# Kernel tuning notes

Hardware: AMD Instinct MI355X
Metric: run time of the kernel (lower is better)

The kernel has to match this reference:

```python
import jax, jax.numpy as jnp
import numpy as np

EMBED = 1024
HEADS = 16
HEAD_DIM = EMBED // HEADS
N, SEQ = 8, 1024


def setup_inputs() -> dict:
    key = jax.random.key(0)
    ks = jax.random.split(key, 9)
    values = jax.random.normal(ks[0], (N, SEQ, EMBED), dtype=jnp.float32)
    keys_ = jax.random.normal(ks[1], (N, SEQ, EMBED), dtype=jnp.float32)
    query = jax.random.normal(ks[2], (N, SEQ, EMBED), dtype=jnp.float32)
    mask = jax.random.randint(ks[3], (N, 1, SEQ, SEQ), 0, 2, dtype=jnp.int32)
    s = 1.0 / np.sqrt(HEAD_DIM)
    Wv = jax.random.normal(ks[4], (HEAD_DIM, HEAD_DIM), dtype=jnp.float32) * s
    Wk = jax.random.normal(ks[5], (HEAD_DIM, HEAD_DIM), dtype=jnp.float32) * s
    Wq = jax.random.normal(ks[6], (HEAD_DIM, HEAD_DIM), dtype=jnp.float32) * s
    Wo = jax.random.normal(ks[7], (EMBED, EMBED), dtype=jnp.float32) * (1.0 / np.sqrt(EMBED))
    bo = jax.random.normal(ks[8], (EMBED,), dtype=jnp.float32) * 0.01
    return {"values": values, "keys": keys_, "query": query, "mask": mask,
            "Wv": Wv, "Wk": Wk, "Wq": Wq, "Wo": Wo, "bo": bo}


def reference(values, keys, query, mask, Wv, Wk, Wq, Wo, bo):
    n, q_len = query.shape[0], query.shape[1]
    v_len, k_len = values.shape[1], keys.shape[1]
    # reshape to (N, len, H, Dh); per-head linear projections share a (Dh,Dh) weight.
    v = values.reshape(n, v_len, HEADS, HEAD_DIM)
    k = keys.reshape(n, k_len, HEADS, HEAD_DIM)
    q = query.reshape(n, q_len, HEADS, HEAD_DIM)
    # torch Linear: x @ W.T
    v = jnp.einsum('nlhd,ed->nlhe', v, Wv)
    k = jnp.einsum('nlhd,ed->nlhe', k, Wk)
    q = jnp.einsum('nlhd,ed->nlhe', q, Wq)
    # scores (N,H,Q,K); mask BEFORE scaling, exactly as the torch module does
    att = jnp.einsum('nqhd,nkhd->nhqk', q, k)
    att = jnp.where(mask == 0, jnp.float32(-1e20), att)
    att = jax.nn.softmax(att / jnp.sqrt(jnp.float32(EMBED)), axis=3)
    out = jnp.einsum('nhql,nlhd->nqhd', att, v).reshape(n, q_len, EMBED)
    return out @ Wo.T + bo
```

## Files before the change

### kernel.cpp

```cpp
#include <hip/hip_runtime.h>
#include <hip/hip_bf16.h>

using bf16x8 = __attribute__((ext_vector_type(8))) __bf16;
using f32x4  = __attribute__((ext_vector_type(4))) float;
using f32x2  = __attribute__((ext_vector_type(2))) float;

#define NB 8
#define SEQ 1024
#define HEADS 16
#define HD 64
#define EMB 1024

#if __has_builtin(__builtin_amdgcn_exp2f)
  #define EXPD(x) __builtin_amdgcn_exp2f(x)
  #define QSCALE  0.04508422f
#else
  #define EXPD(x) __expf(x)
  #define QSCALE  0.03125f
#endif

__device__ __forceinline__ int cvtpk_bf16(float lo, float hi) {
    int r;
    asm("v_cvt_pk_bf16_f32 %0, %1, %2" : "=v"(r) : "v"(lo), "v"(hi));
    return r;
}

__device__ __forceinline__ float sel0(float e, unsigned long long m) {
    float r;
    asm("v_cndmask_b32 %0, 0, %1, %2" : "=v"(r) : "v"(e), "s"(m));
    return r;
}

__device__ __forceinline__ void gld16(const __bf16* g, __bf16* l) {
    __builtin_amdgcn_global_load_lds((const __attribute__((address_space(1))) void*)g,
                                     (__attribute__((address_space(3))) void*)l, 16, 0, 0);
}

__global__ __launch_bounds__(256) void mask_perm(const int* __restrict__ mask,
                                                 unsigned long long* __restrict__ mq)
{
    const int t = threadIdx.x, w = t >> 6, lane = t & 63, quad = lane >> 4, lq = lane & 15;
    const int bx = blockIdx.x;
    const int n = blockIdx.y;
    const int qg = bx >> 5, g = (bx >> 4) & 1, kc = bx & 15;
    const int q = qg * 128 + g * 64 + w * 16 + lq;
    const int* mrow = mask + ((size_t)n * SEQ + q) * SEQ + kc * 64 + quad * 4;
    unsigned long long* dst = mq + ((size_t)(((n * 8 + qg) * 4 + w) * 2 + g) * 16 + kc) * 16;
    #pragma unroll
    for (int kt = 0; kt < 4; ++kt)
        #pragma unroll
        for (int r = 0; r < 4; ++r) {
            unsigned long long b = __ballot(mrow[kt * 16 + r] != 0);
            if (lane == 0) dst[kt * 4 + r] = b;
        }
}

__global__ __launch_bounds__(256, 4) void proj_mfma(
    const float* __restrict__ q_in, const float* __restrict__ k_in, const float* __restrict__ v_in,
    const float* __restrict__ Wq, const float* __restrict__ Wk, const float* __restrict__ Wv,
    __bf16* __restrict__ qp, __bf16* __restrict__ kp, __bf16* __restrict__ vpt)
{
    const int z = blockIdx.z;
    const float* X  = (z == 0) ? q_in : (z == 1) ? k_in : v_in;
    const float* Wf = (z == 0) ? Wq   : (z == 1) ? Wk   : Wv;

    __shared__ __align__(16) __bf16 Wb[64 * 72];
    __shared__ __align__(16) __bf16 Xb[64 * 72];
    const int t = threadIdx.x;
    const int nh = blockIdx.y, n = nh >> 4, h = nh & 15;
    const int l0 = blockIdx.x * 64;
    for (int i = t; i < 4096; i += 256)
        Wb[(i >> 6) * 72 + (i & 63)] = (__bf16)Wf[i];
    {
        const int row = t >> 2, seg = (t & 3) * 16;
        const float* src = X + ((size_t)(n * SEQ + l0 + row)) * EMB + h * 64 + seg;
        union { __bf16 b[16]; uint4 u[2]; } tmp;
        #pragma unroll
        for (int jj = 0; jj < 4; ++jj) {
            float4 f = ((const float4*)src)[jj];
            tmp.b[jj*4+0] = (__bf16)f.x; tmp.b[jj*4+1] = (__bf16)f.y;
            tmp.b[jj*4+2] = (__bf16)f.z; tmp.b[jj*4+3] = (__bf16)f.w;
        }
        *(uint4*)&Xb[row * 72 + seg]     = tmp.u[0];
        *(uint4*)&Xb[row * 72 + seg + 8] = tmp.u[1];
    }
    __syncthreads();
    const int w = t >> 6, lane = t & 63, quad = lane >> 4, lr = lane & 15;
    bf16x8 af[2];
    #pragma unroll
    for (int ks = 0; ks < 2; ++ks)
        af[ks] = *(const bf16x8*)&Xb[(w * 16 + lr) * 72 + ks * 32 + quad * 8];
    const f32x4 zero4 = {0.f, 0.f, 0.f, 0.f};
    f32x4 acc[4];
    #pragma unroll
    for (int et = 0; et < 4; ++et) {
        acc[et] = zero4;
        #pragma unroll
        for (int ks = 0; ks < 2; ++ks) {
            bf16x8 bfrag = *(const bf16x8*)&Wb[(et * 16 + lr) * 72 + ks * 32 + quad * 8];
            acc[et] = __builtin_amdgcn_mfma_f32_16x16x32_bf16(af[ks], bfrag, acc[et], 0, 0, 0);
        }
    }
    if (z == 0) {
        #pragma unroll
        for (int et = 0; et < 4; ++et) acc[et] *= QSCALE;
    }
    __syncthreads();
    if (z < 2) {
        #pragma unroll
        for (int et = 0; et < 4; ++et)
            #pragma unroll
            for (int rr = 0; rr < 4; ++rr)
                Xb[(w * 16 + quad * 4 + rr) * 72 + et * 16 + lr] = (__bf16)acc[et][rr];
        __syncthreads();
        const int row = t >> 2, seg = (t & 3) * 16;
        uint4 a = *(uint4*)&Xb[row * 72 + seg];
        uint4 b = *(uint4*)&Xb[row * 72 + seg + 8];
        __bf16* outp = (z == 0) ? qp : kp;
        __bf16* dst = outp + (size_t)nh * 65536 + (size_t)(l0 + row) * 64 + seg;
        *(uint4*)&dst[0] = a;
        *(uint4*)&dst[8] = b;
    } else {
        #pragma unroll
        for (int et = 0; et < 4; ++et)
            #pragma unroll
            for (int rr = 0; rr < 4; ++rr)
                Xb[(et * 16 + lr) * 72 + w * 16 + quad * 4 + rr] = (__bf16)acc[et][rr];
        __syncthreads();
        const int e = t >> 2, seg = (t & 3) * 16;
        uint4 a = *(uint4*)&Xb[e * 72 + seg];
        uint4 b = *(uint4*)&Xb[e * 72 + seg + 8];
        __bf16* dst = vpt + (size_t)nh * 65536 + (size_t)e * SEQ + l0 + seg;
        *(uint4*)&dst[0] = a;
        *(uint4*)&dst[8] = b;
    }
}

__global__ __launch_bounds__(256, 4) void attn_mfma(
    const __bf16* __restrict__ qp, const __bf16* __restrict__ kp, const __bf16* __restrict__ vpt,
    const unsigned long long* __restrict__ mq, __bf16* __restrict__ attn_out)
{
    __shared__ __align__(16) __bf16 KV[2][2][64 * 64];
    const int t = threadIdx.x, w = t >> 6, lane = t & 63, quad = lane >> 4, lr = lane & 15;
    const int bid = blockIdx.x;
    const int nh = bid & 127, qg = bid >> 7;
    const int n = nh >> 4, h = nh & 15;
    const int q0 = qg * 128;
    const __bf16* Q  = qp  + (size_t)nh * 65536;
    const __bf16* K  = kp  + (size_t)nh * 65536;
    const __bf16* VT = vpt + (size_t)nh * 65536;

    const int wu = __builtin_amdgcn_readfirstlane(w);
    const unsigned long long* mq_w = mq + (size_t)((n * 8 + qg) * 4 + wu) * 512;

    int qrow[2];
    bf16x8 qf[2][2];
    #pragma unroll
    for (int g = 0; g < 2; ++g) {
        qrow[g] = q0 + g * 64 + w * 16 + lr;
        qf[g][0] = *(const bf16x8*)&Q[(size_t)qrow[g] * 64 + quad * 8];
        qf[g][1] = *(const bf16x8*)&Q[(size_t)qrow[g] * 64 + 32 + quad * 8];
    }

    const int srow = t >> 3, sc8 = t & 7;
    const int sswz = (sc8 ^ (srow & 7)) * 8;
    const int kofs = srow * 64 + sswz;
    const int vofs = srow * SEQ + sswz;

    auto issue = [&](int kc) {
        const int b = kc & 1;
        __bf16* kb = (__bf16*)&KV[b][0][0];
        __bf16* vb = (__bf16*)&KV[b][1][0];
        const __bf16* ksrc = K  + (size_t)kc * 4096 + kofs;
        const __bf16* vsrc = VT + (size_t)kc * 64   + vofs;
        gld16(ksrc,            kb + t * 8);
        gld16(ksrc + 32 * 64,  kb + t * 8 + 2048);
        gld16(vsrc,            vb + t * 8);
        gld16(vsrc + 32 * SEQ, vb + t * 8 + 2048);
    };

    const int s0 = ((quad ^ (lr & 7))) * 8;
    const int s1 = s0 ^ 32;

    const f32x4 zero4 = {0.f, 0.f, 0.f, 0.f};
    f32x4 O[2][4];
    #pragma unroll
    for (int g = 0; g < 2; ++g)
        #pragma unroll
        for (int mt = 0; mt < 4; ++mt) O[g][mt] = zero4;
    f32x2 lp2[2] = {{0.f, 0.f}, {0.f, 0.f}};

    issue(0);
    for (int kc = 0; kc < 16; ++kc) {
        __syncthreads();
        if (kc + 1 < 16) issue(kc + 1);
        const __bf16* Kb = (const __bf16*)&KV[kc & 1][0][0];
        const __bf16* Vb = (const __bf16*)&KV[kc & 1][1][0];

        f32x4 S[2][4];
        #pragma unroll
        for (int g = 0; g < 2; ++g)
            #pragma unroll
            for (int kt = 0; kt < 4; ++kt) S[g][kt] = zero4;
        __builtin_amdgcn_s_setprio(1);
        #pragma unroll
        for (int kt = 0; kt < 4; ++kt) {
            bf16x8 kf0 = *(const bf16x8*)&Kb[(kt * 16 + lr) * 64 + s0];
            bf16x8 kf1 = *(const bf16x8*)&Kb[(kt * 16 + lr) * 64 + s1];
            S[0][kt] = __builtin_amdgcn_mfma_f32_16x16x32_bf16(kf0, qf[0][0], S[0][kt], 0, 0, 0);
            S[1][kt] = __builtin_amdgcn_mfma_f32_16x16x32_bf16(kf0, qf[1][0], S[1][kt], 0, 0, 0);
            S[0][kt] = __builtin_amdgcn_mfma_f32_16x16x32_bf16(kf1, qf[0][1], S[0][kt], 0, 0, 0);
            S[1][kt] = __builtin_amdgcn_mfma_f32_16x16x32_bf16(kf1, qf[1][1], S[1][kt], 0, 0, 0);
        }
        __builtin_amdgcn_s_setprio(0);

        bf16x8 pf[2][2];
        #pragma unroll
        for (int g = 0; g < 2; ++g) {
            const unsigned long long* Mg = mq_w + g * 256 + kc * 16;
            float ev[16];
            #pragma unroll
            for (int kt = 0; kt < 4; ++kt)
                #pragma unroll
                for (int r = 0; r < 4; ++r)
                    ev[kt * 4 + r] = sel0(EXPD(S[g][kt][r]), Mg[kt * 4 + r]);
            #pragma unroll
            for (int i = 0; i < 8; ++i) {
                f32x2 p2 = {ev[2 * i], ev[2 * i + 1]};
                lp2[g] += p2;
            }
            #pragma unroll
            for (int ks = 0; ks < 2; ++ks) {
                const int ka = (2 * ks) * 4, kb2 = (2 * ks + 1) * 4;
                int d0 = cvtpk_bf16(ev[ka + 0], ev[ka + 1]);
                int d1 = cvtpk_bf16(ev[ka + 2], ev[ka + 3]);
                int d2 = cvtpk_bf16(ev[kb2 + 0], ev[kb2 + 1]);
                int d3 = cvtpk_bf16(ev[kb2 + 2], ev[kb2 + 3]);
                asm("v_permlane32_swap_b32 %0, %1" : "+v"(d0), "+v"(d2));
                asm("v_permlane16_swap_b32 %0, %1" : "+v"(d0), "+v"(d2));
                asm("v_permlane32_swap_b32 %0, %1" : "+v"(d1), "+v"(d3));
                asm("v_permlane16_swap_b32 %0, %1" : "+v"(d1), "+v"(d3));
                union { int di[4]; bf16x8 v; } pb;
                pb.di[0] = d0; pb.di[1] = d1; pb.di[2] = d2; pb.di[3] = d3;
                pf[g][ks] = pb.v;
            }
        }

        __builtin_amdgcn_s_setprio(1);
        #pragma unroll
        for (int ks = 0; ks < 2; ++ks) {
            const int sv = ks ? s1 : s0;
            #pragma unroll
            for (int mt = 0; mt < 4; ++mt) {
                bf16x8 vf = *(const bf16x8*)&Vb[(mt * 16 + lr) * 64 + sv];
                O[0][mt] = __builtin_amdgcn_mfma_f32_16x16x32_bf16(vf, pf[0][ks], O[0][mt], 0, 0, 0);
                O[1][mt] = __builtin_amdgcn_mfma_f32_16x16x32_bf16(vf, pf[1][ks], O[1][mt], 0, 0, 0);
            }
        }
        __builtin_amdgcn_s_setprio(0);
    }
    #pragma unroll
    for (int g = 0; g < 2; ++g) {
        float l = lp2[g].x + lp2[g].y;
        l += __shfl_xor(l, 16, 64);
        l += __shfl_xor(l, 32, 64);
        const float linv = 1.0f / l;
        #pragma unroll
        for (int mt = 0; mt < 4; ++mt) {
            union { __bf16 b[4]; uint2 u; } pk;
            #pragma unroll
            for (int r = 0; r < 4; ++r) pk.b[r] = (__bf16)(O[g][mt][r] * linv);
            *(uint2*)&attn_out[((size_t)n * SEQ + qrow[g]) * EMB + h * 64 + mt * 16 + quad * 4] = pk.u;
        }
    }
}

__global__ __launch_bounds__(256) void cvt_wo(const float* __restrict__ Wo, __bf16* __restrict__ Wob)
{
    int i = blockIdx.x * 256 + threadIdx.x;
    float4 f = *(const float4*)&Wo[(size_t)i * 4];
    union { __bf16 b[4]; uint2 u; } tmp;
    tmp.b[0] = (__bf16)f.x; tmp.b[1] = (__bf16)f.y; tmp.b[2] = (__bf16)f.z; tmp.b[3] = (__bf16)f.w;
    *(uint2*)&Wob[(size_t)i * 4] = tmp.u;
}

__global__ __launch_bounds__(256, 4) void out_gemm_mfma(
    const __bf16* __restrict__ A, const __bf16* __restrict__ B,
    const float* __restrict__ bo, float* __restrict__ out)
{
    __shared__ __align__(16) __bf16 As[64 * 40];
    __shared__ __align__(16) __bf16 Bs[128 * 40];
    const int t = threadIdx.x, w = t >> 6, lane = t & 63, quad = lane >> 4, lr = lane & 15;
    const int wr = (w >> 1) * 32, wc = (w & 1) * 64;
    const int r0 = blockIdx.y * 64, e0 = blockIdx.x * 128;
    const f32x4 zero4 = {0.f, 0.f, 0.f, 0.f};
    f32x4 acc[2][4];
    #pragma unroll
    for (int mt = 0; mt < 2; ++mt)
        #pragma unroll
        for (int nt = 0; nt < 4; ++nt) acc[mt][nt] = zero4;
    for (int k0 = 0; k0 < 1024; k0 += 32) {
        __syncthreads();
        {
            int row = t >> 2, c8 = t & 3;
            *(uint4*)&As[row * 40 + c8 * 8] =
                *(const uint4*)&A[(size_t)(r0 + row) * EMB + k0 + c8 * 8];
        }
        for (int c = t; c < 512; c += 256) {
            int row = c >> 2, c8 = c & 3;
            *(uint4*)&Bs[row * 40 + c8 * 8] =
                *(const uint4*)&B[(size_t)(e0 + row) * EMB + k0 + c8 * 8];
        }
        __syncthreads();
        bf16x8 af[2], bf[4];
        #pragma unroll
        for (int mt = 0; mt < 2; ++mt)
            af[mt] = *(const bf16x8*)&As[(wr + mt * 16 + lr) * 40 + quad * 8];
        #pragma unroll
        for (int nt = 0; nt < 4; ++nt)
            bf[nt] = *(const bf16x8*)&Bs[(wc + nt * 16 + lr) * 40 + quad * 8];
        #pragma unroll
        for (int mt = 0; mt < 2; ++mt)
            #pragma unroll
            for (int nt = 0; nt < 4; ++nt)
                acc[mt][nt] = __builtin_amdgcn_mfma_f32_16x16x32_bf16(af[mt], bf[nt], acc[mt][nt], 0, 0, 0);
    }
    float bv[4];
    #pragma unroll
    for (int nt = 0; nt < 4; ++nt) bv[nt] = bo[e0 + wc + nt * 16 + lr];
    #pragma unroll
    for (int mt = 0; mt < 2; ++mt)
        #pragma unroll
        for (int nt = 0; nt < 4; ++nt)
            #pragma unroll
            for (int rr = 0; rr < 4; ++rr)
                out[(size_t)(r0 + wr + mt * 16 + quad * 4 + rr) * EMB + e0 + wc + nt * 16 + lr] =
                    acc[mt][nt][rr] + bv[nt];
}

extern "C" void kernel_launch(void* const* d_in, const int* in_sizes, int n_in,
                              void* d_out, int out_size, void* d_ws, size_t ws_size,
                              hipStream_t stream) {
    const float* values = (const float*)d_in[0];
    const float* keys   = (const float*)d_in[1];
    const float* query  = (const float*)d_in[2];
    const int*   mask   = (const int*)d_in[3];
    const float* Wv     = (const float*)d_in[4];
    const float* Wk     = (const float*)d_in[5];
    const float* Wq     = (const float*)d_in[6];
    const float* Wo     = (const float*)d_in[7];
    const float* bo     = (const float*)d_in[8];
    float* out = (float*)d_out;

    const size_t per = (size_t)NB * HEADS * SEQ * HD;
    __bf16* qp   = (__bf16*)d_ws;
    __bf16* kp   = qp + per;
    __bf16* vpt  = kp + per;
    __bf16* attn = vpt + per;
    __bf16* Wob  = attn + (size_t)NB * SEQ * EMB;
    unsigned long long* maskq = (unsigned long long*)(Wob + (size_t)EMB * EMB);

    mask_perm<<<dim3(256, NB), 256, 0, stream>>>(mask, maskq);
    proj_mfma<<<dim3(16, 128, 3), 256, 0, stream>>>(query, keys, values, Wq, Wk, Wv, qp, kp, vpt);
    cvt_wo<<<1024, 256, 0, stream>>>(Wo, Wob);
    attn_mfma<<<1024, 256, 0, stream>>>(qp, kp, vpt, maskq, attn);
    out_gemm_mfma<<<dim3(EMB / 128, NB * SEQ / 64), 256, 0, stream>>>(attn, Wob, bo, out);
}
```

Before: 278.2 us.

## Stage mask via LDS, compute softmax row sums with MFMA, pipeline output GEMM

The mask_perm kernel now loads a 128x64 int tile into shared memory with coalesced 16-byte loads before doing the ballots, replacing strided per-lane global reads and halving the grid. In the attention kernel, softmax row sums are accumulated with an extra MFMA against a ones vector instead of vector adds plus cross-lane shuffles, and the zero-init of S is folded into the first MFMA. The output GEMM switches to double-buffered, swizzled direct global-to-LDS loads with a K-step of 64 and lowers occupancy to 3 blocks per CU. Summing the bf16-rounded probabilities changes the normalization slightly, and the larger LDS footprint reduces occupancy.

```diff
diff --git a/kernel.cpp b/kernel.cpp
--- a/kernel.cpp
+++ b/kernel.cpp
@@ -3,7 +3,6 @@
 
 using bf16x8 = __attribute__((ext_vector_type(8))) __bf16;
 using f32x4  = __attribute__((ext_vector_type(4))) float;
-using f32x2  = __attribute__((ext_vector_type(2))) float;
 
 #define NB 8
 #define SEQ 1024
@@ -39,20 +38,30 @@
 __global__ __launch_bounds__(256) void mask_perm(const int* __restrict__ mask,
                                                  unsigned long long* __restrict__ mq)
 {
+    __shared__ __align__(16) int Ms[128 * 68];
     const int t = threadIdx.x, w = t >> 6, lane = t & 63, quad = lane >> 4, lq = lane & 15;
-    const int bx = blockIdx.x;
     const int n = blockIdx.y;
-    const int qg = bx >> 5, g = (bx >> 4) & 1, kc = bx & 15;
-    const int q = qg * 128 + g * 64 + w * 16 + lq;
-    const int* mrow = mask + ((size_t)n * SEQ + q) * SEQ + kc * 64 + quad * 4;
-    unsigned long long* dst = mq + ((size_t)(((n * 8 + qg) * 4 + w) * 2 + g) * 16 + kc) * 16;
-    #pragma unroll
-    for (int kt = 0; kt < 4; ++kt)
-        #pragma unroll
-        for (int r = 0; r < 4; ++r) {
-            unsigned long long b = __ballot(mrow[kt * 16 + r] != 0);
-            if (lane == 0) dst[kt * 4 + r] = b;
-        }
+    const int qg = blockIdx.x >> 4, kc = blockIdx.x & 15;
+    const int* src = mask + ((size_t)n * SEQ + qg * 128) * SEQ + kc * 64;
+    #pragma unroll
+    for (int i = 0; i < 8; ++i) {
+        const int c = t + i * 256, row = c >> 4, seg = c & 15;
+        uint4 v = *(const uint4*)&src[(size_t)row * SEQ + seg * 4];
+        *(uint4*)&Ms[row * 68 + seg * 4] = v;
+    }
+    __syncthreads();
+    #pragma unroll
+    for (int g = 0; g < 2; ++g) {
+        const int row = (g * 64 + w * 16 + lq) * 68 + quad * 4;
+        unsigned long long* dst = mq + ((size_t)(((n * 8 + qg) * 4 + w) * 2 + g) * 16 + kc) * 16;
+        #pragma unroll
+        for (int kt = 0; kt < 4; ++kt)
+            #pragma unroll
+            for (int r = 0; r < 4; ++r) {
+                unsigned long long b = __ballot(Ms[row + kt * 16 + r] != 0);
+                if (lane == 0) dst[kt * 4 + r] = b;
+            }
+    }
 }
 
 __global__ __launch_bounds__(256, 4) void proj_mfma(
@@ -162,6 +171,10 @@
         qf[g][1] = *(const bf16x8*)&Q[(size_t)qrow[g] * 64 + 32 + quad * 8];
     }
 
+    bf16x8 onesf;
+    #pragma unroll
+    for (int i = 0; i < 8; ++i) onesf[i] = (__bf16)1.0f;
+
     const int srow = t >> 3, sc8 = t & 7;
     const int sswz = (sc8 ^ (srow & 7)) * 8;
     const int kofs = srow * 64 + sswz;
@@ -184,11 +197,13 @@
 
     const f32x4 zero4 = {0.f, 0.f, 0.f, 0.f};
     f32x4 O[2][4];
-    #pragma unroll
-    for (int g = 0; g < 2; ++g)
+    f32x4 Lacc[2];
+    #pragma unroll
+    for (int g = 0; g < 2; ++g) {
+        Lacc[g] = zero4;
         #pragma unroll
         for (int mt = 0; mt < 4; ++mt) O[g][mt] = zero4;
-    f32x2 lp2[2] = {{0.f, 0.f}, {0.f, 0.f}};
+    }
 
     issue(0);
     for (int kc = 0; kc < 16; ++kc) {
@@ -198,17 +213,13 @@
         const __bf16* Vb = (const __bf16*)&KV[kc & 1][1][0];
 
         f32x4 S[2][4];
-        #pragma unroll
-        for (int g = 0; g < 2; ++g)
-            #pragma unroll
-            for (int kt = 0; kt < 4; ++kt) S[g][kt] = zero4;
         __builtin_amdgcn_s_setprio(1);
         #pragma unroll
         for (int kt = 0; kt < 4; ++kt) {
             bf16x8 kf0 = *(const bf16x8*)&Kb[(kt * 16 + lr) * 64 + s0];
             bf16x8 kf1 = *(const bf16x8*)&Kb[(kt * 16 + lr) * 64 + s1];
-            S[0][kt] = __builtin_amdgcn_mfma_f32_16x16x32_bf16(kf0, qf[0][0], S[0][kt], 0, 0, 0);
-            S[1][kt] = __builtin_amdgcn_mfma_f32_16x16x32_bf16(kf0, qf[1][0], S[1][kt], 0, 0, 0);
+            S[0][kt] = __builtin_amdgcn_mfma_f32_16x16x32_bf16(kf0, qf[0][0], zero4, 0, 0, 0);
+            S[1][kt] = __builtin_amdgcn_mfma_f32_16x16x32_bf16(kf0, qf[1][0], zero4, 0, 0, 0);
             S[0][kt] = __builtin_amdgcn_mfma_f32_16x16x32_bf16(kf1, qf[0][1], S[0][kt], 0, 0, 0);
             S[1][kt] = __builtin_amdgcn_mfma_f32_16x16x32_bf16(kf1, qf[1][1], S[1][kt], 0, 0, 0);
         }
@@ -224,11 +235,6 @@
                 #pragma unroll
                 for (int r = 0; r < 4; ++r)
                     ev[kt * 4 + r] = sel0(EXPD(S[g][kt][r]), Mg[kt * 4 + r]);
-            #pragma unroll
-            for (int i = 0; i < 8; ++i) {
-                f32x2 p2 = {ev[2 * i], ev[2 * i + 1]};
-                lp2[g] += p2;
-            }
             #pragma unroll
             for (int ks = 0; ks < 2; ++ks) {
                 const int ka = (2 * ks) * 4, kb2 = (2 * ks + 1) * 4;
@@ -250,6 +256,8 @@
         #pragma unroll
         for (int ks = 0; ks < 2; ++ks) {
             const int sv = ks ? s1 : s0;
+            Lacc[0] = __builtin_amdgcn_mfma_f32_16x16x32_bf16(onesf, pf[0][ks], Lacc[0], 0, 0, 0);
+            Lacc[1] = __builtin_amdgcn_mfma_f32_16x16x32_bf16(onesf, pf[1][ks], Lacc[1], 0, 0, 0);
             #pragma unroll
             for (int mt = 0; mt < 4; ++mt) {
                 bf16x8 vf = *(const bf16x8*)&Vb[(mt * 16 + lr) * 64 + sv];
@@ -261,10 +269,7 @@
     }
     #pragma unroll
     for (int g = 0; g < 2; ++g) {
-        float l = lp2[g].x + lp2[g].y;
-        l += __shfl_xor(l, 16, 64);
-        l += __shfl_xor(l, 32, 64);
-        const float linv = 1.0f / l;
+        const float linv = 1.0f / Lacc[g][0];
         #pragma unroll
         for (int mt = 0; mt < 4; ++mt) {
             union { __bf16 b[4]; uint2 u; } pk;
@@ -284,46 +289,61 @@
     *(uint2*)&Wob[(size_t)i * 4] = tmp.u;
 }
 
-__global__ __launch_bounds__(256, 4) void out_gemm_mfma(
+__global__ __launch_bounds__(256, 3) void out_gemm_mfma(
     const __bf16* __restrict__ A, const __bf16* __restrict__ B,
     const float* __restrict__ bo, float* __restrict__ out)
 {
-    __shared__ __align__(16) __bf16 As[64 * 40];
-    __shared__ __align__(16) __bf16 Bs[128 * 40];
+    __shared__ __align__(16) __bf16 AB[2][(64 + 128) * 64];
     const int t = threadIdx.x, w = t >> 6, lane = t & 63, quad = lane >> 4, lr = lane & 15;
     const int wr = (w >> 1) * 32, wc = (w & 1) * 64;
     const int r0 = blockIdx.y * 64, e0 = blockIdx.x * 128;
+
+    const int srow = t >> 3, sj = t & 7;
+    const int sswz = (sj ^ (srow & 7)) * 8;
+
+    auto issue = [&](int st) {
+        __bf16* buf = (__bf16*)&AB[st & 1][0];
+        const __bf16* as = A + (size_t)(r0 + srow) * EMB + st * 64 + sswz;
+        const __bf16* bs = B + (size_t)(e0 + srow) * EMB + st * 64 + sswz;
+        gld16(as,            buf + t * 8);
+        gld16(as + 32 * EMB, buf + t * 8 + 2048);
+        gld16(bs,            buf + 4096 + t * 8);
+        gld16(bs + 32 * EMB, buf + 4096 + t * 8 + 2048);
+        gld16(bs + 64 * EMB, buf + 4096 + t * 8 + 4096);
+        gld16(bs + 96 * EMB, buf + 4096 + t * 8 + 6144);
+    };
+
+    const int s0 = (quad ^ (lr & 7)) * 8, s1 = s0 ^ 32;
     const f32x4 zero4 = {0.f, 0.f, 0.f, 0.f};
     f32x4 acc[2][4];
     #pragma unroll
     for (int mt = 0; mt < 2; ++mt)
         #pragma unroll
         for (int nt = 0; nt < 4; ++nt) acc[mt][nt] = zero4;
-    for (int k0 = 0; k0 < 1024; k0 += 32) {
+
+    issue(0);
+    for (int st = 0; st < 16; ++st) {
         __syncthreads();
-        {
-            int row = t >> 2, c8 = t & 3;
-            *(uint4*)&As[row * 40 + c8 * 8] =
-                *(const uint4*)&A[(size_t)(r0 + row) * EMB + k0 + c8 * 8];
-        }
-        for (int c = t; c < 512; c += 256) {
-            int row = c >> 2, c8 = c & 3;
-            *(uint4*)&Bs[row * 40 + c8 * 8] =
-                *(const uint4*)&B[(size_t)(e0 + row) * EMB + k0 + c8 * 8];
-        }
-        __syncthreads();
-        bf16x8 af[2], bf[4];
-        #pragma unroll
-        for (int mt = 0; mt < 2; ++mt)
-            af[mt] = *(const bf16x8*)&As[(wr + mt * 16 + lr) * 40 + quad * 8];
-        #pragma unroll
-        for (int nt = 0; nt < 4; ++nt)
-            bf[nt] = *(const bf16x8*)&Bs[(wc + nt * 16 + lr) * 40 + quad * 8];
-        #pragma unroll
-        for (int mt = 0; mt < 2; ++mt)
+        if (st + 1 < 16) issue(st + 1);
+        const __bf16* buf = (const __bf16*)&AB[st & 1][0];
+        #pragma unroll
+        for (int ks = 0; ks < 2; ++ks) {
+            const int sv = ks ? s1 : s0;
+            bf16x8 af[2], bf[4];
+            #pragma unroll
+            for (int mt = 0; mt < 2; ++mt)
+                af[mt] = *(const bf16x8*)&buf[(wr + mt * 16 + lr) * 64 + sv];
             #pragma unroll
             for (int nt = 0; nt < 4; ++nt)
-                acc[mt][nt] = __builtin_amdgcn_mfma_f32_16x16x32_bf16(af[mt], bf[nt], acc[mt][nt], 0, 0, 0);
+                bf[nt] = *(const bf16x8*)&buf[4096 + (wc + nt * 16 + lr) * 64 + sv];
+            __builtin_amdgcn_s_setprio(1);
+            #pragma unroll
+            for (int mt = 0; mt < 2; ++mt)
+                #pragma unroll
+                for (int nt = 0; nt < 4; ++nt)
+                    acc[mt][nt] = __builtin_amdgcn_mfma_f32_16x16x32_bf16(af[mt], bf[nt], acc[mt][nt], 0, 0, 0);
+            __builtin_amdgcn_s_setprio(0);
+        }
     }
     float bv[4];
     #pragma unroll
@@ -360,7 +380,7 @@
     __bf16* Wob  = attn + (size_t)NB * SEQ * EMB;
     unsigned long long* maskq = (unsigned long long*)(Wob + (size_t)EMB * EMB);
 
-    mask_perm<<<dim3(256, NB), 256, 0, stream>>>(mask, maskq);
+    mask_perm<<<dim3(128, NB), 256, 0, stream>>>(mask, maskq);
     proj_mfma<<<dim3(16, 128, 3), 256, 0, stream>>>(query, keys, values, Wq, Wk, Wv, qp, kp, vpt);
     cvt_wo<<<1024, 256, 0, stream>>>(Wo, Wob);
     attn_mfma<<<1024, 256, 0, stream>>>(qp, kp, vpt, maskq, attn);
```

Measured after the change: 254.7 us. -8.4%, faster.
